# Kernel tuning notes

Measured on AMD Instinct MI355X. Metric: run time of the kernel, lower is better.

The kernel has to match this reference:

```python
import jax, jax.numpy as jnp
import numpy as np

N_NODES = 100000
N_EDGES = 1600000
N_GRAPHS = 512
IN_DIM = 3
HIDDEN = 128


def setup_inputs() -> dict:
    key = jax.random.key(0)
    ks = jax.random.split(key, 8)
    x = jax.random.normal(ks[0], (N_NODES, IN_DIM), dtype=jnp.float32)
    edge_index = jax.random.randint(ks[1], (2, N_EDGES), 0, N_NODES, dtype=jnp.int64)
    batch = jnp.sort(jax.random.randint(ks[2], (N_NODES,), 0, N_GRAPHS, dtype=jnp.int64))
    W1 = jax.random.normal(ks[3], (IN_DIM, HIDDEN), dtype=jnp.float32) / np.sqrt(IN_DIM)
    b1 = jnp.zeros((HIDDEN,), dtype=jnp.float32)
    W2 = jax.random.normal(ks[4], (HIDDEN, HIDDEN), dtype=jnp.float32) / np.sqrt(HIDDEN)
    b2 = jnp.zeros((HIDDEN,), dtype=jnp.float32)
    Wc = jax.random.normal(ks[5], (HIDDEN, 1), dtype=jnp.float32) / np.sqrt(HIDDEN)
    bc = jnp.zeros((1,), dtype=jnp.float32)
    return {"x": x, "edge_index": edge_index, "batch": batch,
            "W1": W1, "b1": b1, "W2": W2, "b2": b2, "Wc": Wc, "bc": bc}


def _gcn_conv(x, W, b, src, dst, n_nodes):
    # PyG GCNConv: h = X W; add self-loops; symmetric norm D^-1/2 (A+I) D^-1/2; scatter-add; + bias
    h = x @ W  # [N, H]
    deg = jax.ops.segment_sum(jnp.ones_like(dst, dtype=h.dtype), dst, num_segments=n_nodes) + 1.0  # +1 self-loop
    dinv = jax.lax.rsqrt(deg)  # [N]
    norm = dinv[src] * dinv[dst]  # [E]
    msg = h[src] * norm[:, None]  # [E, H] gather + scale
    agg = jax.ops.segment_sum(msg, dst, num_segments=n_nodes)  # scatter-add
    agg = agg + h * (dinv * dinv)[:, None]  # self-loop contribution
    return agg + b


def reference(x, edge_index, batch, W1, b1, W2, b2, Wc, bc):
    src, dst = edge_index[0], edge_index[1]
    n = x.shape[0]
    h = jax.nn.relu(_gcn_conv(x, W1, b1, src, dst, n))
    h = jax.nn.relu(_gcn_conv(h, W2, b2, src, dst, n))
    # global mean pool over graphs
    sums = jax.ops.segment_sum(h, batch, num_segments=N_GRAPHS)  # [G, H]
    cnt = jax.ops.segment_sum(jnp.ones((n,), dtype=h.dtype), batch, num_segments=N_GRAPHS)
    pooled = sums / jnp.maximum(cnt, 1.0)[:, None]
    logits = pooled @ Wc + bc  # [G, 1]
    return jax.nn.sigmoid(logits).squeeze(-1)  # [G]
```

## Files before the change

### kernel.cpp

```cpp
#include <hip/hip_runtime.h>
#include <hip/hip_bf16.h>
#include <math.h>

#define H 128
#define NTPB 256
#define NBKT 256
#define BSH 9
#define BMSK 511
#define EPB 8192
#define POOL_CHUNK 2048
#define SRC_MASK 0x1FFFFu
#define NPW 8

typedef __attribute__((ext_vector_type(8))) short short8;
typedef __attribute__((ext_vector_type(4))) float floatx4;
typedef __attribute__((ext_vector_type(2))) float f2v;

__device__ __forceinline__ void atomAddF(float* p, float v) {
    __hip_atomic_fetch_add(p, v, __ATOMIC_RELAXED, __HIP_MEMORY_SCOPE_AGENT);
}

__device__ __forceinline__ short f2bf(float v) {
    __hip_bfloat16 b = __float2bfloat16(v);
    return __builtin_bit_cast(short, b);
}

__device__ __forceinline__ f2v splat2(float v) { return (f2v){v, v}; }

__global__ void hist_kernel(const int* __restrict__ ei, int E, int* __restrict__ ghist,
                            const float* __restrict__ W2, __hip_bfloat16* __restrict__ Bp,
                            int EB) {
    int t = threadIdx.x;
    if (blockIdx.x >= EB) {
        int idx = (blockIdx.x - EB) * NTPB + t;
        if (idx < 2048) {
            int frag = idx >> 6, lane = idx & 63;
            int nt = frag >> 2, c = frag & 3, quad = lane >> 4, m16 = lane & 15;
#pragma unroll
            for (int jj = 0; jj < 8; jj++) {
                int k = c * 32 + quad * 8 + jj;
                Bp[idx * 8 + jj] = __float2bfloat16(W2[k * H + nt * 16 + m16]);
            }
        }
        return;
    }
    __shared__ int lh[NBKT];
    lh[t] = 0;
    __syncthreads();
    int base = blockIdx.x * EPB;
#pragma unroll
    for (int k = 0; k < EPB / NTPB; k++) {
        int e = base + k * NTPB + t;
        if (e < E) atomicAdd(&lh[((unsigned)ei[E + e]) >> BSH], 1);
    }
    __syncthreads();
    if (lh[t]) atomicAdd(&ghist[t], lh[t]);
}

__global__ void scan_buckets(const int* __restrict__ ghist, int* __restrict__ gbase,
                             int* __restrict__ gcursor) {
    __shared__ int sd[NBKT];
    int t = threadIdx.x;
    int v = ghist[t];
    sd[t] = v; __syncthreads();
    for (int s = 1; s < NBKT; s <<= 1) {
        int u = (t >= s) ? sd[t - s] : 0;
        __syncthreads();
        sd[t] += u;
        __syncthreads();
    }
    int ex = sd[t] - v;
    gbase[t] = ex;
    gcursor[t] = ex;
    if (t == NBKT - 1) gbase[NBKT] = sd[t];
}

__global__ void partition_kernel(const int* __restrict__ ei, int E,
                                 int* __restrict__ gcursor, unsigned* __restrict__ ebuf) {
    __shared__ int lcur[NBKT];
    __shared__ int lbase[NBKT];
    int t = threadIdx.x;
    lcur[t] = 0;
    __syncthreads();
    int base = blockIdx.x * EPB;
    unsigned short rk[EPB / NTPB];
#pragma unroll
    for (int k = 0; k < EPB / NTPB; k++) {
        int e = base + k * NTPB + t;
        rk[k] = 0;
        if (e < E) rk[k] = (unsigned short)atomicAdd(&lcur[((unsigned)ei[E + e]) >> BSH], 1);
    }
    __syncthreads();
    lbase[t] = atomicAdd(&gcursor[t], lcur[t]);
    __syncthreads();
#pragma unroll
    for (int k = 0; k < EPB / NTPB; k++) {
        int e = base + k * NTPB + t;
        if (e < E) {
            unsigned d = (unsigned)ei[E + e];
            unsigned s = (unsigned)ei[e];
            ebuf[lbase[d >> BSH] + rk[k]] = ((d & BMSK) << 17) | s;
        }
    }
}

__global__ void bucket_sort(const unsigned* __restrict__ ebuf, const int* __restrict__ gbase,
                            const float* __restrict__ x,
                            int* __restrict__ rowptr, unsigned* __restrict__ csr,
                            float4* __restrict__ xs4, int N) {
    __shared__ int ldeg[512];
    __shared__ int loff[512];
    __shared__ int sd[NTPB];
    int t = threadIdx.x, b = blockIdx.x;
    int node0 = b << BSH;
    int beg = gbase[b], end = gbase[b + 1];
    ldeg[t] = 0; ldeg[t + 256] = 0;
    __syncthreads();
    for (int i = beg + t; i < end; i += NTPB)
        atomicAdd(&ldeg[ebuf[i] >> 17], 1);
    __syncthreads();
    int d0 = ldeg[2 * t], d1 = ldeg[2 * t + 1];
    int ps = d0 + d1;
    sd[t] = ps; __syncthreads();
    for (int s = 1; s < NTPB; s <<= 1) {
        int u = (t >= s) ? sd[t - s] : 0;
        __syncthreads();
        sd[t] += u;
        __syncthreads();
    }
    int ex = sd[t] - ps;
    loff[2 * t] = ex;
    loff[2 * t + 1] = ex + d0;
    __syncthreads();
    for (int i = t; i < 512; i += NTPB) {
        int node = node0 + i;
        if (node < N) {
            rowptr[node] = beg + loff[i];
            float dv = rsqrtf((float)(ldeg[i] + 1));
            xs4[node] = make_float4(x[3 * node] * dv, x[3 * node + 1] * dv,
                                    x[3 * node + 2] * dv, dv);
        } else if (node == N) {
            rowptr[N] = beg + loff[i];
        }
    }
    __syncthreads();
    for (int i = beg + t; i < end; i += NTPB) {
        unsigned u = ebuf[i];
        int pos = beg + atomicAdd(&loff[u >> 17], 1);
        csr[pos] = u & 0x1FFFFu;
    }
}

__global__ void l1_gather(const float4* __restrict__ xs4,
                          const int* __restrict__ rowptr, const unsigned* __restrict__ csr,
                          float4* __restrict__ aggx4, int N) {
    int n = blockIdx.x * blockDim.x + threadIdx.x;
    if (n >= N) return;
    float4 xn = xs4[n];
    float a0 = xn.x, a1 = xn.y, a2 = xn.z;
    int beg = rowptr[n], end = rowptr[n + 1];
    int i = beg;
    for (; i + 4 <= end; i += 4) {
        float4 q0 = xs4[csr[i]];
        float4 q1 = xs4[csr[i + 1]];
        float4 q2 = xs4[csr[i + 2]];
        float4 q3 = xs4[csr[i + 3]];
        a0 += q0.x + q1.x + q2.x + q3.x;
        a1 += q0.y + q1.y + q2.y + q3.y;
        a2 += q0.z + q1.z + q2.z + q3.z;
    }
    for (; i < end; ++i) {
        float4 q = xs4[csr[i]];
        a0 += q.x; a1 += q.y; a2 += q.z;
    }
    float dv = xn.w;
    aggx4[n] = make_float4(a0 * dv, a1 * dv, a2 * dv, dv);
}

__device__ __forceinline__ void edge_accs(float px, float py, float pz, float pw,
                                          const f2v wa, const f2v wb, const f2v wc,
                                          const f2v bb, f2v& acc) {
    f2v z = __builtin_elementwise_fma(splat2(px), wa, bb);
    z = __builtin_elementwise_fma(splat2(py), wb, z);
    z = __builtin_elementwise_fma(splat2(pz), wc, z);
    z = __builtin_elementwise_max(z, (f2v){0.f, 0.f});
    acc = __builtin_elementwise_fma(splat2(pw), z, acc);
}

__global__ void l2_gather(
        const float4* __restrict__ aggx4,
        const int* __restrict__ rowptr, const unsigned* __restrict__ csr,
        const float* __restrict__ W1, const float* __restrict__ b1,
        __hip_bfloat16* __restrict__ agg1, int N) {
    __shared__ float4 sbuf[NTPB / 64][2][64];
    __shared__ float4 sown[NTPB / 64][NPW];
    int t = threadIdx.x;
    int lane = t & 63;
    int w = t >> 6;
    int n0 = (blockIdx.x * (NTPB / 64) + w) * NPW;
    if (n0 >= N) return;
    int k0 = 2 * lane;
    f2v wa = *(const f2v*)&W1[k0];
    f2v wb = *(const f2v*)&W1[H + k0];
    f2v wc = *(const f2v*)&W1[2 * H + k0];
    f2v bb = *(const f2v*)&b1[k0];
    int rp[NPW + 1];
#pragma unroll
    for (int nd = 0; nd <= NPW; nd++) rp[nd] = rowptr[min(n0 + nd, N)];
    if (lane < NPW) sown[w][lane] = aggx4[min(n0 + lane, N - 1)];
    f2v accs[NPW];
#pragma unroll
    for (int nd = 0; nd < NPW; nd++) accs[nd] = (f2v){0.f, 0.f};
    int beg = rp[0], end = rp[NPW];
    if (beg < end) {
        sbuf[w][0][lane] = aggx4[csr[beg + lane] & SRC_MASK];
    }
    unsigned cB = csr[beg + 64 + lane];
    int cur = 0;
    for (int win = beg; win < end; win += 64) {
        int nwin = win + 64;
        float4 rn;
        bool have_next = nwin < end;
        if (have_next) rn = aggx4[cB & SRC_MASK];
        unsigned cNN = csr[win + 128 + lane];
        int wend = min(nwin, end);
#pragma unroll
        for (int nd = 0; nd < NPW; nd++) {
            int s = max(rp[nd], win);
            int e2 = min(rp[nd + 1], wend);
            int e = s;
            for (; e + 4 <= e2; e += 4) {
                float4 p0 = sbuf[w][cur][e - win];
                float4 p1 = sbuf[w][cur][e - win + 1];
                float4 p2 = sbuf[w][cur][e - win + 2];
                float4 p3 = sbuf[w][cur][e - win + 3];
                edge_accs(p0.x, p0.y, p0.z, p0.w, wa, wb, wc, bb, accs[nd]);
                edge_accs(p1.x, p1.y, p1.z, p1.w, wa, wb, wc, bb, accs[nd]);
                edge_accs(p2.x, p2.y, p2.z, p2.w, wa, wb, wc, bb, accs[nd]);
                edge_accs(p3.x, p3.y, p3.z, p3.w, wa, wb, wc, bb, accs[nd]);
            }
            for (; e < e2; ++e) {
                float4 p = sbuf[w][cur][e - win];
                edge_accs(p.x, p.y, p.z, p.w, wa, wb, wc, bb, accs[nd]);
            }
        }
        if (have_next) sbuf[w][cur ^ 1][lane] = rn;
        cB = cNN;
        cur ^= 1;
    }
#pragma unroll
    for (int nd = 0; nd < NPW; nd++) {
        int n = n0 + nd;
        if (n < N) {
            float4 own = sown[w][nd];
            edge_accs(own.x, own.y, own.z, own.w, wa, wb, wc, bb, accs[nd]);
            f2v r = accs[nd] * splat2(own.w);
            unsigned packed = ((unsigned)(unsigned short)f2bf(r.x)) |
                              ((unsigned)(unsigned short)f2bf(r.y) << 16);
            ((unsigned*)agg1)[(size_t)n * (H / 2) + lane] = packed;
        }
    }
}

__global__ __launch_bounds__(NTPB, 4) void gemm_nodedot(
        const __hip_bfloat16* __restrict__ agg1, const __hip_bfloat16* __restrict__ Bp,
        const float* __restrict__ b2, const float* __restrict__ Wc,
        float* __restrict__ nodedot, int N) {
    __shared__ float sb2[H];
    __shared__ float swc[H];
    int t = threadIdx.x;
    if (t < H) { sb2[t] = b2[t]; swc[t] = Wc[t]; }
    __syncthreads();
    int wave = t >> 6, lane = t & 63;
    int quad = lane >> 4, m16 = lane & 15;
    int tile = blockIdx.x * 4 + wave;
    int rowbase = tile * 16;
    if (rowbase >= N) return;
    int m = rowbase + m16;
    const short8* as8 = (const short8*)agg1;
    short8 af[4];
    if (m < N) {
#pragma unroll
        for (int c = 0; c < 4; c++) af[c] = as8[(size_t)m * 16 + c * 4 + quad];
    } else {
#pragma unroll
        for (int c = 0; c < 4; c++) af[c] = (short8){0, 0, 0, 0, 0, 0, 0, 0};
    }
    const short8* bp = (const short8*)Bp;
    floatx4 acc[8];
#pragma unroll
    for (int nt = 0; nt < 8; nt++) acc[nt] = (floatx4){0.f, 0.f, 0.f, 0.f};
#pragma unroll
    for (int nt = 0; nt < 8; nt++) {
#pragma unroll
        for (int c = 0; c < 4; c++) {
            short8 bf = bp[(nt * 4 + c) * 64 + lane];
            acc[nt] = __builtin_amdgcn_mfma_f32_16x16x32_bf16(af[c], bf, acc[nt], 0, 0, 0);
        }
    }
    float dot0 = 0.f, dot1 = 0.f, dot2 = 0.f, dot3 = 0.f;
#pragma unroll
    for (int nt = 0; nt < 8; nt++) {
        int col = nt * 16 + m16;
        float bcol = sb2[col], wcol = swc[col];
        dot0 += fmaxf(acc[nt][0] + bcol, 0.f) * wcol;
        dot1 += fmaxf(acc[nt][1] + bcol, 0.f) * wcol;
        dot2 += fmaxf(acc[nt][2] + bcol, 0.f) * wcol;
        dot3 += fmaxf(acc[nt][3] + bcol, 0.f) * wcol;
    }
#pragma unroll
    for (int s = 1; s < 16; s <<= 1) {
        dot0 += __shfl_xor(dot0, s);
        dot1 += __shfl_xor(dot1, s);
        dot2 += __shfl_xor(dot2, s);
        dot3 += __shfl_xor(dot3, s);
    }
    if (m16 < 4) {
        int row = rowbase + quad * 4 + m16;
        if (row < N) {
            float d = (m16 == 0) ? dot0 : (m16 == 1) ? dot1 : (m16 == 2) ? dot2 : dot3;
            nodedot[row] = d;
        }
    }
}

__global__ void pool_kernel(const float* __restrict__ nodedot, const int* __restrict__ batch,
                            float* __restrict__ gsum, int* __restrict__ gcnt, int N, int G) {
    extern __shared__ char sm[];
    float* ls = (float*)sm;
    int*   lc = (int*)(sm + (size_t)G * sizeof(float));
    int t = threadIdx.x;
    for (int g = t; g < G; g += blockDim.x) { ls[g] = 0.f; lc[g] = 0; }
    __syncthreads();
    int base = blockIdx.x * POOL_CHUNK;
    int endn = min(base + POOL_CHUNK, N);
    for (int n = base + t; n < endn; n += blockDim.x) {
        int g = batch[n];
        atomicAdd(&ls[g], nodedot[n]);
        atomicAdd(&lc[g], 1);
    }
    __syncthreads();
    for (int g = t; g < G; g += blockDim.x) {
        if (lc[g] != 0) {
            atomAddF(&gsum[g], ls[g]);
            atomicAdd(&gcnt[g], lc[g]);
        }
    }
}

__global__ void out_kernel(const float* __restrict__ gsum, const int* __restrict__ gcnt,
                           const float* __restrict__ bc, float* __restrict__ out, int G) {
    int g = blockIdx.x * blockDim.x + threadIdx.x;
    if (g >= G) return;
    float c = fmaxf((float)gcnt[g], 1.f);
    float logit = gsum[g] / c + bc[0];
    out[g] = 1.f / (1.f + expf(-logit));
}

extern "C" void kernel_launch(void* const* d_in, const int* in_sizes, int n_in,
                              void* d_out, int out_size, void* d_ws, size_t ws_size,
                              hipStream_t stream) {
    const float* x     = (const float*)d_in[0];
    const int*   ei    = (const int*)d_in[1];
    const int*   batch = (const int*)d_in[2];
    const float* W1    = (const float*)d_in[3];
    const float* b1    = (const float*)d_in[4];
    const float* W2    = (const float*)d_in[5];
    const float* b2    = (const float*)d_in[6];
    const float* Wc    = (const float*)d_in[7];
    const float* bc    = (const float*)d_in[8];
    float* out = (float*)d_out;

    int N = in_sizes[2];
    int E = in_sizes[1] / 2;
    int G = out_size;

    char* ws = (char*)d_ws;
    size_t off = 0;
    auto alloc = [&](size_t bytes) {
        void* p = ws + off;
        off += (bytes + 255) & ~(size_t)255;
        return p;
    };
    __hip_bfloat16* agg1 = (__hip_bfloat16*)alloc((size_t)N * H * sizeof(__hip_bfloat16));
    float4* xs4   = (float4*)alloc((size_t)N * sizeof(float4));
    float4* aggx4 = (float4*)alloc((size_t)(SRC_MASK + 1) * sizeof(float4));
    float* nodedot= (float*)alloc((size_t)N * sizeof(float));
    float* gsum   = (float*)alloc((size_t)G * sizeof(float));
    int*   gcnt   = (int*)  alloc((size_t)G * sizeof(int));
    int*   ghist  = (int*)  alloc((size_t)NBKT * sizeof(int));
    char*  zero_end = ws + off;
    int*   gbase  = (int*)  alloc((size_t)(NBKT + 1) * sizeof(int));
    int*   gcursor= (int*)  alloc((size_t)NBKT * sizeof(int));
    int*   rowptr = (int*)  alloc((size_t)(N + 1) * sizeof(int));
    unsigned* csr = (unsigned*)alloc((size_t)(E + 256) * sizeof(unsigned));
    unsigned* ebuf= (unsigned*)alloc((size_t)E * sizeof(unsigned));
    __hip_bfloat16* Bp = (__hip_bfloat16*)alloc((size_t)H * H * sizeof(__hip_bfloat16));

    (void)hipMemsetAsync(gsum, 0, (size_t)(zero_end - (char*)gsum), stream);

    int EB = (E + EPB - 1) / EPB;
    hist_kernel<<<EB + 8, NTPB, 0, stream>>>(ei, E, ghist, W2, Bp, EB);
    scan_buckets<<<1, NBKT, 0, stream>>>(ghist, gbase, gcursor);
    partition_kernel<<<EB, NTPB, 0, stream>>>(ei, E, gcursor, ebuf);
    {
        int nbs = (N >> BSH) + 1;
        bucket_sort<<<nbs, NTPB, 0, stream>>>(ebuf, gbase, x, rowptr, csr, xs4, N);
    }

    l1_gather<<<(N + NTPB - 1) / NTPB, NTPB, 0, stream>>>(xs4, rowptr, csr, aggx4, N);

    {
        int npb = NPW * (NTPB / 64);
        int blocks = (N + npb - 1) / npb;
        l2_gather<<<blocks, NTPB, 0, stream>>>(aggx4, rowptr, csr, W1, b1, agg1, N);
    }

    {
        int ntiles = (N + 15) / 16;
        gemm_nodedot<<<(ntiles + 3) / 4, NTPB, 0, stream>>>(agg1, Bp, b2, Wc, nodedot, N);
    }

    {
        int pblocks = (N + POOL_CHUNK - 1) / POOL_CHUNK;
        size_t smem = (size_t)G * (sizeof(float) + sizeof(int));
        pool_kernel<<<pblocks, NTPB, smem, stream>>>(nodedot, batch, gsum, gcnt, N, G);
    }

    out_kernel<<<(G + NTPB - 1) / NTPB, NTPB, 0, stream>>>(gsum, gcnt, bc, out, G);
}
```

Before: 209.1 us.

## Split wave into four edge groups in layer-2 gather with shuffle reduction

Restructures l2_gather so each wave's 64 lanes form 4 groups of 16. Each lane now handles 8 hidden features instead of 2, and the 4 groups process 4 edges in parallel; partial sums are combined with cross-lane shuffles before a single 16-byte bf16 store per lane group. Nodes per wave drop from 8 to 4, which doubles the number of waves. The aim is to cut the serial per-edge loop length and the average degree-dependent imbalance, at the cost of more registers, shuffle work and padded iterations when a node's edge count is not a multiple of 4.

```diff
diff --git a/kernel.cpp b/kernel.cpp
--- a/kernel.cpp
+++ b/kernel.cpp
@@ -10,7 +10,7 @@
 #define EPB 8192
 #define POOL_CHUNK 2048
 #define SRC_MASK 0x1FFFFu
-#define NPW 8
+#define NPW 4
 
 typedef __attribute__((ext_vector_type(8))) short short8;
 typedef __attribute__((ext_vector_type(4))) float floatx4;
@@ -177,16 +177,6 @@
     aggx4[n] = make_float4(a0 * dv, a1 * dv, a2 * dv, dv);
 }
 
-__device__ __forceinline__ void edge_accs(float px, float py, float pz, float pw,
-                                          const f2v wa, const f2v wb, const f2v wc,
-                                          const f2v bb, f2v& acc) {
-    f2v z = __builtin_elementwise_fma(splat2(px), wa, bb);
-    z = __builtin_elementwise_fma(splat2(py), wb, z);
-    z = __builtin_elementwise_fma(splat2(pz), wc, z);
-    z = __builtin_elementwise_max(z, (f2v){0.f, 0.f});
-    acc = __builtin_elementwise_fma(splat2(pw), z, acc);
-}
-
 __global__ void l2_gather(
         const float4* __restrict__ aggx4,
         const int* __restrict__ rowptr, const unsigned* __restrict__ csr,
@@ -197,24 +187,30 @@
     int t = threadIdx.x;
     int lane = t & 63;
     int w = t >> 6;
+    int g = lane >> 4;
+    int j = lane & 15;
     int n0 = (blockIdx.x * (NTPB / 64) + w) * NPW;
     if (n0 >= N) return;
-    int k0 = 2 * lane;
-    f2v wa = *(const f2v*)&W1[k0];
-    f2v wb = *(const f2v*)&W1[H + k0];
-    f2v wc = *(const f2v*)&W1[2 * H + k0];
-    f2v bb = *(const f2v*)&b1[k0];
+    f2v wa[4], wb[4], wc[4], bb[4];
+#pragma unroll
+    for (int q = 0; q < 4; q++) {
+        int k0 = 8 * j + 2 * q;
+        wa[q] = *(const f2v*)&W1[k0];
+        wb[q] = *(const f2v*)&W1[H + k0];
+        wc[q] = *(const f2v*)&W1[2 * H + k0];
+        bb[q] = *(const f2v*)&b1[k0];
+    }
     int rp[NPW + 1];
 #pragma unroll
     for (int nd = 0; nd <= NPW; nd++) rp[nd] = rowptr[min(n0 + nd, N)];
     if (lane < NPW) sown[w][lane] = aggx4[min(n0 + lane, N - 1)];
-    f2v accs[NPW];
-#pragma unroll
-    for (int nd = 0; nd < NPW; nd++) accs[nd] = (f2v){0.f, 0.f};
+    f2v accs[NPW][4];
+#pragma unroll
+    for (int nd = 0; nd < NPW; nd++)
+#pragma unroll
+        for (int q = 0; q < 4; q++) accs[nd][q] = (f2v){0.f, 0.f};
     int beg = rp[0], end = rp[NPW];
-    if (beg < end) {
-        sbuf[w][0][lane] = aggx4[csr[beg + lane] & SRC_MASK];
-    }
+    if (beg < end) sbuf[w][0][lane] = aggx4[csr[beg + lane] & SRC_MASK];
     unsigned cB = csr[beg + 64 + lane];
     int cur = 0;
     for (int win = beg; win < end; win += 64) {
@@ -228,20 +224,19 @@
         for (int nd = 0; nd < NPW; nd++) {
             int s = max(rp[nd], win);
             int e2 = min(rp[nd + 1], wend);
-            int e = s;
-            for (; e + 4 <= e2; e += 4) {
-                float4 p0 = sbuf[w][cur][e - win];
-                float4 p1 = sbuf[w][cur][e - win + 1];
-                float4 p2 = sbuf[w][cur][e - win + 2];
-                float4 p3 = sbuf[w][cur][e - win + 3];
-                edge_accs(p0.x, p0.y, p0.z, p0.w, wa, wb, wc, bb, accs[nd]);
-                edge_accs(p1.x, p1.y, p1.z, p1.w, wa, wb, wc, bb, accs[nd]);
-                edge_accs(p2.x, p2.y, p2.z, p2.w, wa, wb, wc, bb, accs[nd]);
-                edge_accs(p3.x, p3.y, p3.z, p3.w, wa, wb, wc, bb, accs[nd]);
-            }
-            for (; e < e2; ++e) {
-                float4 p = sbuf[w][cur][e - win];
-                edge_accs(p.x, p.y, p.z, p.w, wa, wb, wc, bb, accs[nd]);
+            for (int e = s; e < e2; e += 4) {
+                int eg = e + g;
+                int idx = min(eg, e2 - 1) - win;
+                float4 p = sbuf[w][cur][idx];
+                float pw = (eg < e2) ? p.w : 0.f;
+#pragma unroll
+                for (int q = 0; q < 4; q++) {
+                    f2v z = __builtin_elementwise_fma(splat2(p.x), wa[q], bb[q]);
+                    z = __builtin_elementwise_fma(splat2(p.y), wb[q], z);
+                    z = __builtin_elementwise_fma(splat2(p.z), wc[q], z);
+                    z = __builtin_elementwise_max(z, (f2v){0.f, 0.f});
+                    accs[nd][q] = __builtin_elementwise_fma(splat2(pw), z, accs[nd][q]);
+                }
             }
         }
         if (have_next) sbuf[w][cur ^ 1][lane] = rn;
@@ -251,14 +246,24 @@
 #pragma unroll
     for (int nd = 0; nd < NPW; nd++) {
         int n = n0 + nd;
-        if (n < N) {
-            float4 own = sown[w][nd];
-            edge_accs(own.x, own.y, own.z, own.w, wa, wb, wc, bb, accs[nd]);
-            f2v r = accs[nd] * splat2(own.w);
-            unsigned packed = ((unsigned)(unsigned short)f2bf(r.x)) |
-                              ((unsigned)(unsigned short)f2bf(r.y) << 16);
-            ((unsigned*)agg1)[(size_t)n * (H / 2) + lane] = packed;
-        }
+        if (n >= N) continue;
+        float4 own = sown[w][nd];
+        short8 o;
+#pragma unroll
+        for (int q = 0; q < 4; q++) {
+            f2v v = accs[nd][q];
+            v.x += __shfl_xor(v.x, 16); v.y += __shfl_xor(v.y, 16);
+            v.x += __shfl_xor(v.x, 32); v.y += __shfl_xor(v.y, 32);
+            f2v z = __builtin_elementwise_fma(splat2(own.x), wa[q], bb[q]);
+            z = __builtin_elementwise_fma(splat2(own.y), wb[q], z);
+            z = __builtin_elementwise_fma(splat2(own.z), wc[q], z);
+            z = __builtin_elementwise_max(z, (f2v){0.f, 0.f});
+            v = __builtin_elementwise_fma(splat2(own.w), z, v);
+            v = v * splat2(own.w);
+            o[2 * q] = f2bf(v.x);
+            o[2 * q + 1] = f2bf(v.y);
+        }
+        if (g == 0) *(short8*)(&agg1[(size_t)n * H + 8 * j]) = o;
     }
 }
 
```

Measured after the change: 217.8 us. +4.2%, slower.
